# Optimization experiments

Hardware: AMD Instinct MI355X
Metric: run time of the kernel (lower is better)

## Reference

```python
import jax, jax.numpy as jnp
import numpy as np

H = 1024
I = 4096
E = 8
B, S, K = 2, 2048, 2


def setup_inputs() -> dict:
    key = jax.random.key(0)
    k1, k2, k3, k4, k5, k6 = jax.random.split(key, 6)
    x = jax.random.normal(k1, (B, S, H), dtype=jnp.float32)
    expert_indices = jax.random.randint(k2, (B, S, K), 0, E, dtype=jnp.int32)
    expert_weights = jax.random.uniform(k3, (B, S, K), dtype=jnp.float32)
    gate_proj = jax.random.normal(k4, (E, I, H), dtype=jnp.float32) * 0.02
    up_proj = jax.random.normal(k5, (E, I, H), dtype=jnp.float32) * 0.02
    down_proj = jax.random.normal(k6, (E, H, I), dtype=jnp.float32) * 0.02
    return {"x": x, "expert_indices": expert_indices, "expert_weights": expert_weights,
            "gate_proj": gate_proj, "up_proj": up_proj, "down_proj": down_proj}


def reference(x, expert_indices, expert_weights, gate_proj, up_proj, down_proj):
    b, s, h = x.shape
    e = gate_proj.shape[0]
    k = expert_indices.shape[-1]
    xf = x.reshape(-1, h)                       # [N, H]
    idx = expert_indices.reshape(-1, k)         # [N, K]
    wts = expert_weights.reshape(-1, k)         # [N, K]
    # combine[n, e] = sum over slots k with idx[n,k]==e of wts[n,k]
    onehot = jax.nn.one_hot(idx, e, dtype=x.dtype)            # [N, K, E]
    combine = jnp.einsum('nk,nke->ne', wts, onehot)           # [N, E]
    out = jnp.zeros_like(xf)
    # Fixed small unrolled loop over experts (data dims fully vectorized).
    for ei in range(e):
        gate = jax.nn.silu(xf @ gate_proj[ei].T)              # [N, I]
        up = xf @ up_proj[ei].T                               # [N, I]
        out = out + ((gate * up) @ down_proj[ei].T) * combine[:, ei:ei + 1]
    return out.reshape(b, s, h)
```

## Files before the change

### kernel.cpp

```cpp
#include <hip/hip_runtime.h>
#include <hip/hip_bf16.h>
#include <cstdint>

#define HD 1024
#define ID 4096
#define NE 8
#define NTOK 4096
#define NASS 8192
#define NWL 72

typedef unsigned short u16;
typedef __attribute__((ext_vector_type(8))) __bf16 bf16x8;
typedef __attribute__((ext_vector_type(4))) float f32x4;

__device__ __forceinline__ void async16(void* lds, const void* g) {
  __builtin_amdgcn_global_load_lds(
      (const __attribute__((address_space(1))) uint32_t*)g,
      (__attribute__((address_space(3))) uint32_t*)lds, 16, 0, 0);
}

__device__ __forceinline__ u16 f2b(float f) {
  __bf16 h = (__bf16)f;
  return __builtin_bit_cast(u16, h);
}

__device__ __forceinline__ bf16x8 cvt8(const float* p) {
  const float4* q = (const float4*)p;
  float4 a = q[0], b = q[1];
  bf16x8 v;
  v[0] = (__bf16)a.x; v[1] = (__bf16)a.y; v[2] = (__bf16)a.z; v[3] = (__bf16)a.w;
  v[4] = (__bf16)b.x; v[5] = (__bf16)b.y; v[6] = (__bf16)b.z; v[7] = (__bf16)b.w;
  return v;
}

__device__ __forceinline__ void pinned_barrier() {
  __builtin_amdgcn_sched_barrier(0);
  __builtin_amdgcn_s_barrier();
  __builtin_amdgcn_sched_barrier(0);
}

__global__ void k_pre(const float* __restrict__ x, const float* __restrict__ gate,
                      const float* __restrict__ up, u16* __restrict__ xb,
                      u16* __restrict__ wg, u16* __restrict__ wu,
                      float* __restrict__ out) {
  const size_t stride = (size_t)gridDim.x * 256;
  for (size_t v = (size_t)blockIdx.x * 256 + threadIdx.x; v < 8912896ull; v += stride) {
    const float* src; u16* dst; size_t off;
    if (v < 524288ull)        { src = x;    dst = xb; off = v;
      float4 z = {0.f, 0.f, 0.f, 0.f};
      float4* op = (float4*)(out + off * 8);
      op[0] = z; op[1] = z;
    }
    else if (v < 4718592ull)  { src = gate; dst = wg; off = v - 524288ull; }
    else                      { src = up;   dst = wu; off = v - 4718592ull; }
    size_t i8 = off * 8;
    *(bf16x8*)(dst + i8) = cvt8(src + i8);
  }
}

__global__ void k_meta(const int* __restrict__ eidx, int* __restrict__ offsets,
                       int* __restrict__ wl, int* __restrict__ tokl) {
  __shared__ int cnt[NE], offs_s[NE + 1], cur[NE];
  int t = threadIdx.x;
  if (t < NE) cnt[t] = 0;
  __syncthreads();
  for (int i = t; i < NASS; i += 1024) atomicAdd(&cnt[eidx[i]], 1);
  __syncthreads();
  if (t == 0) {
    int s = 0;
    for (int e = 0; e < NE; ++e) { offs_s[e] = s; s += cnt[e]; }
    offs_s[NE] = s;
    int w = 0;
    for (int e = 0; e < NE; ++e)
      for (int mt = 0; mt * 128 < cnt[e]; ++mt) wl[w++] = (e << 16) | mt;
    for (; w < NWL; ++w) wl[w] = -1;
  }
  if (t < NE) cur[t] = 0;
  __syncthreads();
  for (int i = t; i < NASS; i += 1024) {
    int e = eidx[i];
    int p = atomicAdd(&cur[e], 1);
    tokl[offs_s[e] + p] = i;
  }
  if (t <= NE) offsets[t] = offs_s[t];
}

__global__ __launch_bounds__(256, 2) void k_g1(
    const u16* __restrict__ xb, const u16* __restrict__ wg, const u16* __restrict__ wu,
    const float* __restrict__ down, u16* __restrict__ wd,
    const int* __restrict__ offsets, const int* __restrict__ wl,
    const int* __restrict__ tokl, u16* __restrict__ interm) {
  const int bx = blockIdx.x;
  const int t = threadIdx.x;
  if (bx >= 32) {
    int cid = (bx - 32) + 32 * (int)blockIdx.y;
    if (cid < 2048) {
#pragma unroll
      for (int l = 0; l < 8; ++l) {
        size_t i8 = (((size_t)cid * 8 + l) * 256 + t) * 8;
        *(bf16x8*)(wd + i8) = cvt8(down + i8);
      }
    }
    return;
  }
  const int wle = wl[blockIdx.y];
  if (wle < 0) return;
  const int e = wle >> 16;
  const int m0 = (wle & 0xffff) << 7;
  const int offs = offsets[e];
  const int Me = offsets[e + 1] - offs;
  const int n0 = bx * 128;
  const int lane = t & 63, wv = t >> 6;
  const int wm = wv & 1, wn = wv >> 1;

  __shared__ __align__(16) u16 As[2][128 * 32];
  __shared__ __align__(16) u16 Bg[2][128 * 32];
  __shared__ __align__(16) u16 Bu[2][128 * 32];

  const u16* asrc[2];
#pragma unroll
  for (int p = 0; p < 2; ++p) {
    int c = p * 256 + t;
    int r = c >> 2, c8 = (c & 3) * 8;
    int row = m0 + r; if (row > Me - 1) row = Me - 1;
    asrc[p] = xb + (size_t)(tokl[offs + row] >> 1) * HD + c8;
  }
  const u16 *bgsrc[2], *busrc[2];
#pragma unroll
  for (int p = 0; p < 2; ++p) {
    int c = p * 256 + t;
    int r = c >> 2, c8 = (c & 3) * 8;
    size_t boff = ((size_t)e * ID + n0 + r) * HD + c8;
    bgsrc[p] = wg + boff;
    busrc[p] = wu + boff;
  }

#define STAGE1(b, ks)                                                           \
  {                                                                             \
    _Pragma("unroll") for (int p = 0; p < 2; ++p) {                             \
      async16((char*)As[b] + (p * 256 + wv * 64) * 16, asrc[p] + (ks) * 32);    \
      async16((char*)Bg[b] + (p * 256 + wv * 64) * 16, bgsrc[p] + (ks) * 32);   \
      async16((char*)Bu[b] + (p * 256 + wv * 64) * 16, busrc[p] + (ks) * 32);   \
    }                                                                           \
  }

  f32x4 accg[4][4], accu[4][4];
#pragma unroll
  for (int mi = 0; mi < 4; ++mi)
#pragma unroll
    for (int ni = 0; ni < 4; ++ni) {
      accg[mi][ni] = (f32x4){0.f, 0.f, 0.f, 0.f};
      accu[mi][ni] = (f32x4){0.f, 0.f, 0.f, 0.f};
    }

  STAGE1(0, 0);

  const int lrow = lane & 15, lk = (lane >> 4) * 8;
#pragma unroll 1
  for (int ks = 0; ks < HD / 32; ++ks) {
    const int curb = ks & 1;
    if (ks < HD / 32 - 1) {
      STAGE1(curb ^ 1, ks + 1);
      asm volatile("s_waitcnt vmcnt(6)" ::: "memory");
    } else {
      asm volatile("s_waitcnt vmcnt(0)" ::: "memory");
    }
    pinned_barrier();
    bf16x8 af[4], bg[4], bu[4];
#pragma unroll
    for (int mi = 0; mi < 4; ++mi)
      af[mi] = *(const bf16x8*)&As[curb][(wm * 64 + mi * 16 + lrow) * 32 + lk];
#pragma unroll
    for (int ni = 0; ni < 4; ++ni) {
      bg[ni] = *(const bf16x8*)&Bg[curb][(wn * 64 + ni * 16 + lrow) * 32 + lk];
      bu[ni] = *(const bf16x8*)&Bu[curb][(wn * 64 + ni * 16 + lrow) * 32 + lk];
    }
#pragma unroll
    for (int mi = 0; mi < 4; ++mi)
#pragma unroll
      for (int ni = 0; ni < 4; ++ni) {
        accg[mi][ni] = __builtin_amdgcn_mfma_f32_16x16x32_bf16(af[mi], bg[ni], accg[mi][ni], 0, 0, 0);
        accu[mi][ni] = __builtin_amdgcn_mfma_f32_16x16x32_bf16(af[mi], bu[ni], accu[mi][ni], 0, 0, 0);
      }
    pinned_barrier();
  }
#undef STAGE1

#pragma unroll
  for (int mi = 0; mi < 4; ++mi) {
    int rb = wm * 64 + mi * 16 + (lane >> 4) * 4;
#pragma unroll
    for (int ni = 0; ni < 4; ++ni) {
      int col = n0 + wn * 64 + ni * 16 + (lane & 15);
#pragma unroll
      for (int j = 0; j < 4; ++j) {
        int row = m0 + rb + j;
        if (row < Me) {
          float g = accg[mi][ni][j], u = accu[mi][ni][j];
          float s = g / (1.f + __expf(-g));
          interm[(size_t)(offs + row) * ID + col] = f2b(s * u);
        }
      }
    }
  }
}

__global__ __launch_bounds__(256, 2) void k_g2(
    const u16* __restrict__ interm, const u16* __restrict__ wd,
    const int* __restrict__ offsets, const int* __restrict__ wl,
    const int* __restrict__ tokl, const float* __restrict__ ewt,
    float* __restrict__ out) {
  const int wle = wl[blockIdx.y];
  if (wle < 0) return;
  const int e = wle >> 16;
  const int m0 = (wle & 0xffff) << 7;
  const int offs = offsets[e];
  const int Me = offsets[e + 1] - offs;
  const int n0 = blockIdx.x * 256;
  const int t = threadIdx.x, lane = t & 63, wv = t >> 6;
  const int wm = wv & 1, wn = wv >> 1;

  __shared__ __align__(16) u16 As[2][128 * 32];
  __shared__ __align__(16) u16 Bs[2][256 * 32];

  const u16* asrc[2];
#pragma unroll
  for (int p = 0; p < 2; ++p) {
    int c = p * 256 + t;
    int r = c >> 2, c8 = (c & 3) * 8;
    int row = m0 + r; if (row > Me - 1) row = Me - 1;
    asrc[p] = interm + (size_t)(offs + row) * ID + c8;
  }
  const u16* bsrc[4];
#pragma unroll
  for (int p = 0; p < 4; ++p) {
    int c = p * 256 + t;
    int r = c >> 2, c8 = (c & 3) * 8;
    bsrc[p] = wd + ((size_t)e * HD + n0 + r) * ID + c8;
  }

#define STAGE2(b, ks)                                                           \
  {                                                                             \
    _Pragma("unroll") for (int p = 0; p < 2; ++p)                               \
      async16((char*)As[b] + (p * 256 + wv * 64) * 16, asrc[p] + (ks) * 32);    \
    _Pragma("unroll") for (int p = 0; p < 4; ++p)                               \
      async16((char*)Bs[b] + (p * 256 + wv * 64) * 16, bsrc[p] + (ks) * 32);    \
  }

  f32x4 acc[4][8];
#pragma unroll
  for (int mi = 0; mi < 4; ++mi)
#pragma unroll
    for (int ni = 0; ni < 8; ++ni) acc[mi][ni] = (f32x4){0.f, 0.f, 0.f, 0.f};

  STAGE2(0, 0);

  const int lrow = lane & 15, lk = (lane >> 4) * 8;
#pragma unroll 1
  for (int ks = 0; ks < ID / 32; ++ks) {
    const int curb = ks & 1;
    if (ks < ID / 32 - 1) {
      STAGE2(curb ^ 1, ks + 1);
      asm volatile("s_waitcnt vmcnt(6)" ::: "memory");
    } else {
      asm volatile("s_waitcnt vmcnt(0)" ::: "memory");
    }
    pinned_barrier();
    bf16x8 af[4], bfr[8];
#pragma unroll
    for (int mi = 0; mi < 4; ++mi)
      af[mi] = *(const bf16x8*)&As[curb][(wm * 64 + mi * 16 + lrow) * 32 + lk];
#pragma unroll
    for (int ni = 0; ni < 8; ++ni)
      bfr[ni] = *(const bf16x8*)&Bs[curb][(wn * 128 + ni * 16 + lrow) * 32 + lk];
#pragma unroll
    for (int mi = 0; mi < 4; ++mi)
#pragma unroll
      for (int ni = 0; ni < 8; ++ni)
        acc[mi][ni] = __builtin_amdgcn_mfma_f32_16x16x32_bf16(af[mi], bfr[ni], acc[mi][ni], 0, 0, 0);
    pinned_barrier();
  }
#undef STAGE2

#pragma unroll
  for (int mi = 0; mi < 4; ++mi) {
    int rb = wm * 64 + mi * 16 + (lane >> 4) * 4;
#pragma unroll
    for (int j = 0; j < 4; ++j) {
      int row = m0 + rb + j;
      if (row < Me) {
        int aid = tokl[offs + row];
        float w = ewt[aid];
        float* orow = out + (size_t)(aid >> 1) * HD;
#pragma unroll
        for (int ni = 0; ni < 8; ++ni) {
          int col = n0 + wn * 128 + ni * 16 + (lane & 15);
          atomicAdd(orow + col, w * acc[mi][ni][j]);
        }
      }
    }
  }
}

extern "C" void kernel_launch(void* const* d_in, const int* in_sizes, int n_in,
                              void* d_out, int out_size, void* d_ws, size_t ws_size,
                              hipStream_t stream) {
  const float* x    = (const float*)d_in[0];
  const int*   eidx = (const int*)d_in[1];
  const float* ewt  = (const float*)d_in[2];
  const float* gate = (const float*)d_in[3];
  const float* up   = (const float*)d_in[4];
  const float* down = (const float*)d_in[5];
  float* out = (float*)d_out;
  char* ws = (char*)d_ws;

  constexpr size_t OFF_INTERM = 0;
  constexpr size_t OFF_XB     = 67108864;
  constexpr size_t OFF_META   = 75497472;
  constexpr size_t OFF_TOK    = 75498496;
  constexpr size_t OFF_WD     = 75531264;
  constexpr size_t OFF_WG     = 142640128;
  constexpr size_t OFF_WU     = 209748992;

  u16* interm  = (u16*)(ws + OFF_INTERM);
  u16* xb      = (u16*)(ws + OFF_XB);
  int* offsets = (int*)(ws + OFF_META);
  int* wl      = (int*)(ws + OFF_META + 64);
  int* tokl    = (int*)(ws + OFF_TOK);
  u16* wd      = (u16*)(ws + OFF_WD);
  u16* wg      = (u16*)(ws + OFF_WG);
  u16* wu      = (u16*)(ws + OFF_WU);

  k_pre<<<dim3(2048), dim3(256), 0, stream>>>(x, gate, up, xb, wg, wu, out);
  k_meta<<<dim3(1), dim3(1024), 0, stream>>>(eidx, offsets, wl, tokl);
  k_g1<<<dim3(64, NWL), dim3(256), 0, stream>>>(xb, wg, wu, down, wd, offsets, wl, tokl, interm);
  k_g2<<<dim3(HD / 256, NWL), dim3(256), 0, stream>>>(interm, wd, offsets, wl, tokl, ewt, out);
}
```

Measured before the change: 463.9 us.

## Restructure gate/up GEMM to 512 threads, BK=64, swizzled LDS and split MFMA phases

The fused gate/up GEMM kernel now runs 512-thread blocks (8 waves in a 2x4 grid, each computing 64x32), and its K step grows from 32 to 64 with double-buffered LDS. The LDS layout uses an XOR swizzle on 16-byte chunks to avoid bank conflicts, and each K step is split into four barrier-separated MFMA phases with s_setprio raised around the math. The down-projection conversion side-path is re-indexed for the larger block. This aims to raise MFMA utilisation and cut LDS conflicts and per-iteration overhead, at the cost of doubling LDS to 96KB per block, which may limit occupancy, and adding more barriers per K step.

```diff
diff --git a/kernel.cpp b/kernel.cpp
--- a/kernel.cpp
+++ b/kernel.cpp
@@ -38,6 +38,8 @@
   __builtin_amdgcn_s_barrier();
   __builtin_amdgcn_sched_barrier(0);
 }
+
+#define LIDX(row, c8) ((row) * 64 + ((((c8) ^ ((row) & 7))) << 3))
 
 __global__ void k_pre(const float* __restrict__ x, const float* __restrict__ gate,
                       const float* __restrict__ up, u16* __restrict__ xb,
@@ -85,7 +87,7 @@
   if (t <= NE) offsets[t] = offs_s[t];
 }
 
-__global__ __launch_bounds__(256, 2) void k_g1(
+__global__ __launch_bounds__(512, 2) void k_g1(
     const u16* __restrict__ xb, const u16* __restrict__ wg, const u16* __restrict__ wu,
     const float* __restrict__ down, u16* __restrict__ wd,
     const int* __restrict__ offsets, const int* __restrict__ wl,
@@ -94,10 +96,10 @@
   const int t = threadIdx.x;
   if (bx >= 32) {
     int cid = (bx - 32) + 32 * (int)blockIdx.y;
-    if (cid < 2048) {
+    if (cid < 1024) {
 #pragma unroll
       for (int l = 0; l < 8; ++l) {
-        size_t i8 = (((size_t)cid * 8 + l) * 256 + t) * 8;
+        size_t i8 = (((size_t)cid * 8 + l) * 512 + t) * 8;
         *(bf16x8*)(wd + i8) = cvt8(down + i8);
       }
     }
@@ -111,77 +113,115 @@
   const int Me = offsets[e + 1] - offs;
   const int n0 = bx * 128;
   const int lane = t & 63, wv = t >> 6;
-  const int wm = wv & 1, wn = wv >> 1;
-
-  __shared__ __align__(16) u16 As[2][128 * 32];
-  __shared__ __align__(16) u16 Bg[2][128 * 32];
-  __shared__ __align__(16) u16 Bu[2][128 * 32];
+  const int wm = wv >> 2, wn = wv & 3;
+
+  __shared__ __align__(16) u16 As[2][128 * 64];
+  __shared__ __align__(16) u16 Bg[2][128 * 64];
+  __shared__ __align__(16) u16 Bu[2][128 * 64];
 
   const u16* asrc[2];
+  const u16 *bgsrc[2], *busrc[2];
 #pragma unroll
   for (int p = 0; p < 2; ++p) {
-    int c = p * 256 + t;
-    int r = c >> 2, c8 = (c & 3) * 8;
-    int row = m0 + r; if (row > Me - 1) row = Me - 1;
-    asrc[p] = xb + (size_t)(tokl[offs + row] >> 1) * HD + c8;
-  }
-  const u16 *bgsrc[2], *busrc[2];
-#pragma unroll
-  for (int p = 0; p < 2; ++p) {
-    int c = p * 256 + t;
-    int r = c >> 2, c8 = (c & 3) * 8;
-    size_t boff = ((size_t)e * ID + n0 + r) * HD + c8;
+    int c = p * 512 + t;
+    int row = c >> 3;
+    int col8 = (c & 7) ^ (row & 7);
+    int arow = m0 + row; if (arow > Me - 1) arow = Me - 1;
+    asrc[p] = xb + (size_t)(tokl[offs + arow] >> 1) * HD + col8 * 8;
+    size_t boff = ((size_t)e * ID + n0 + row) * HD + col8 * 8;
     bgsrc[p] = wg + boff;
     busrc[p] = wu + boff;
   }
 
-#define STAGE1(b, ks)                                                           \
+#define STAGE1(b, kt)                                                           \
   {                                                                             \
     _Pragma("unroll") for (int p = 0; p < 2; ++p) {                             \
-      async16((char*)As[b] + (p * 256 + wv * 64) * 16, asrc[p] + (ks) * 32);    \
-      async16((char*)Bg[b] + (p * 256 + wv * 64) * 16, bgsrc[p] + (ks) * 32);   \
-      async16((char*)Bu[b] + (p * 256 + wv * 64) * 16, busrc[p] + (ks) * 32);   \
+      async16((char*)As[b] + (p * 512 + wv * 64) * 16, asrc[p] + (kt) * 64);    \
+      async16((char*)Bg[b] + (p * 512 + wv * 64) * 16, bgsrc[p] + (kt) * 64);   \
+      async16((char*)Bu[b] + (p * 512 + wv * 64) * 16, busrc[p] + (kt) * 64);   \
     }                                                                           \
   }
 
-  f32x4 accg[4][4], accu[4][4];
+  f32x4 accg[4][2], accu[4][2];
 #pragma unroll
   for (int mi = 0; mi < 4; ++mi)
 #pragma unroll
-    for (int ni = 0; ni < 4; ++ni) {
+    for (int ni = 0; ni < 2; ++ni) {
       accg[mi][ni] = (f32x4){0.f, 0.f, 0.f, 0.f};
       accu[mi][ni] = (f32x4){0.f, 0.f, 0.f, 0.f};
     }
 
   STAGE1(0, 0);
 
-  const int lrow = lane & 15, lk = (lane >> 4) * 8;
+  const int lr = lane & 15, hi = lane >> 4;
 #pragma unroll 1
-  for (int ks = 0; ks < HD / 32; ++ks) {
-    const int curb = ks & 1;
-    if (ks < HD / 32 - 1) {
-      STAGE1(curb ^ 1, ks + 1);
+  for (int kt = 0; kt < HD / 64; ++kt) {
+    const int cur = kt & 1;
+    if (kt < HD / 64 - 1) {
+      STAGE1(cur ^ 1, kt + 1);
       asm volatile("s_waitcnt vmcnt(6)" ::: "memory");
     } else {
       asm volatile("s_waitcnt vmcnt(0)" ::: "memory");
     }
     pinned_barrier();
-    bf16x8 af[4], bg[4], bu[4];
-#pragma unroll
-    for (int mi = 0; mi < 4; ++mi)
-      af[mi] = *(const bf16x8*)&As[curb][(wm * 64 + mi * 16 + lrow) * 32 + lk];
-#pragma unroll
-    for (int ni = 0; ni < 4; ++ni) {
-      bg[ni] = *(const bf16x8*)&Bg[curb][(wn * 64 + ni * 16 + lrow) * 32 + lk];
-      bu[ni] = *(const bf16x8*)&Bu[curb][(wn * 64 + ni * 16 + lrow) * 32 + lk];
-    }
-#pragma unroll
-    for (int mi = 0; mi < 4; ++mi)
-#pragma unroll
-      for (int ni = 0; ni < 4; ++ni) {
-        accg[mi][ni] = __builtin_amdgcn_mfma_f32_16x16x32_bf16(af[mi], bg[ni], accg[mi][ni], 0, 0, 0);
-        accu[mi][ni] = __builtin_amdgcn_mfma_f32_16x16x32_bf16(af[mi], bu[ni], accu[mi][ni], 0, 0, 0);
-      }
+
+    const u16* A = As[cur];
+    const u16* G = Bg[cur];
+    const u16* U = Bu[cur];
+    bf16x8 af0[4], af1[4], b0[2], b1[2];
+
+#pragma unroll
+    for (int mi = 0; mi < 4; ++mi)
+      af0[mi] = *(const bf16x8*)&A[LIDX(wm * 64 + mi * 16 + lr, hi)];
+#pragma unroll
+    for (int ni = 0; ni < 2; ++ni)
+      b0[ni] = *(const bf16x8*)&G[LIDX(wn * 32 + ni * 16 + lr, hi)];
+    __builtin_amdgcn_s_setprio(1);
+#pragma unroll
+    for (int mi = 0; mi < 4; ++mi)
+#pragma unroll
+      for (int ni = 0; ni < 2; ++ni)
+        accg[mi][ni] = __builtin_amdgcn_mfma_f32_16x16x32_bf16(af0[mi], b0[ni], accg[mi][ni], 0, 0, 0);
+    __builtin_amdgcn_s_setprio(0);
+    pinned_barrier();
+
+#pragma unroll
+    for (int ni = 0; ni < 2; ++ni)
+      b1[ni] = *(const bf16x8*)&U[LIDX(wn * 32 + ni * 16 + lr, hi)];
+    __builtin_amdgcn_s_setprio(1);
+#pragma unroll
+    for (int mi = 0; mi < 4; ++mi)
+#pragma unroll
+      for (int ni = 0; ni < 2; ++ni)
+        accu[mi][ni] = __builtin_amdgcn_mfma_f32_16x16x32_bf16(af0[mi], b1[ni], accu[mi][ni], 0, 0, 0);
+    __builtin_amdgcn_s_setprio(0);
+    pinned_barrier();
+
+#pragma unroll
+    for (int mi = 0; mi < 4; ++mi)
+      af1[mi] = *(const bf16x8*)&A[LIDX(wm * 64 + mi * 16 + lr, 4 + hi)];
+#pragma unroll
+    for (int ni = 0; ni < 2; ++ni)
+      b0[ni] = *(const bf16x8*)&G[LIDX(wn * 32 + ni * 16 + lr, 4 + hi)];
+    __builtin_amdgcn_s_setprio(1);
+#pragma unroll
+    for (int mi = 0; mi < 4; ++mi)
+#pragma unroll
+      for (int ni = 0; ni < 2; ++ni)
+        accg[mi][ni] = __builtin_amdgcn_mfma_f32_16x16x32_bf16(af1[mi], b0[ni], accg[mi][ni], 0, 0, 0);
+    __builtin_amdgcn_s_setprio(0);
+    pinned_barrier();
+
+#pragma unroll
+    for (int ni = 0; ni < 2; ++ni)
+      b1[ni] = *(const bf16x8*)&U[LIDX(wn * 32 + ni * 16 + lr, 4 + hi)];
+    __builtin_amdgcn_s_setprio(1);
+#pragma unroll
+    for (int mi = 0; mi < 4; ++mi)
+#pragma unroll
+      for (int ni = 0; ni < 2; ++ni)
+        accu[mi][ni] = __builtin_amdgcn_mfma_f32_16x16x32_bf16(af1[mi], b1[ni], accu[mi][ni], 0, 0, 0);
+    __builtin_amdgcn_s_setprio(0);
     pinned_barrier();
   }
 #undef STAGE1
@@ -190,8 +230,8 @@
   for (int mi = 0; mi < 4; ++mi) {
     int rb = wm * 64 + mi * 16 + (lane >> 4) * 4;
 #pragma unroll
-    for (int ni = 0; ni < 4; ++ni) {
-      int col = n0 + wn * 64 + ni * 16 + (lane & 15);
+    for (int ni = 0; ni < 2; ++ni) {
+      int col = n0 + wn * 32 + ni * 16 + (lane & 15);
 #pragma unroll
       for (int j = 0; j < 4; ++j) {
         int row = m0 + rb + j;
@@ -333,6 +373,6 @@
 
   k_pre<<<dim3(2048), dim3(256), 0, stream>>>(x, gate, up, xb, wg, wu, out);
   k_meta<<<dim3(1), dim3(1024), 0, stream>>>(eidx, offsets, wl, tokl);
-  k_g1<<<dim3(64, NWL), dim3(256), 0, stream>>>(xb, wg, wu, down, wd, offsets, wl, tokl, interm);
+  k_g1<<<dim3(64, NWL), dim3(512), 0, stream>>>(xb, wg, wu, down, wd, offsets, wl, tokl, interm);
   k_g2<<<dim3(HD / 256, NWL), dim3(256), 0, stream>>>(interm, wd, offsets, wl, tokl, ewt, out);
 }
```

Result: slower. 547.8 us (+18.1%).

## Replace work list with 1D grid interleaving experts and down-proj conversion blocks

Applied to the files above, without the earlier changes.

Removes the serial work-list construction in the metadata kernel and maps a flat 1D block index to (expert, m-tile, n-tile) with the expert as the fastest-varying index. In the first GEMM kernel, down-projection conversion blocks are interleaved with GEMM blocks (5 GEMM chunks to 4 convert chunks) instead of being tacked onto the right half of the grid. The aim is to spread expert work across CUs for better load balance and weight locality, and to overlap the memory-bound conversion with compute. In exchange it assumes at most 10 m-tiles (1280 tokens) per expert, and blocks for empty tiles exit early.

```diff
diff --git a/kernel.cpp b/kernel.cpp
--- a/kernel.cpp
+++ b/kernel.cpp
@@ -7,7 +7,6 @@
 #define NE 8
 #define NTOK 4096
 #define NASS 8192
-#define NWL 72
 
 typedef unsigned short u16;
 typedef __attribute__((ext_vector_type(8))) __bf16 bf16x8;
@@ -59,7 +58,7 @@
 }
 
 __global__ void k_meta(const int* __restrict__ eidx, int* __restrict__ offsets,
-                       int* __restrict__ wl, int* __restrict__ tokl) {
+                       int* __restrict__ tokl) {
   __shared__ int cnt[NE], offs_s[NE + 1], cur[NE];
   int t = threadIdx.x;
   if (t < NE) cnt[t] = 0;
@@ -70,10 +69,6 @@
     int s = 0;
     for (int e = 0; e < NE; ++e) { offs_s[e] = s; s += cnt[e]; }
     offs_s[NE] = s;
-    int w = 0;
-    for (int e = 0; e < NE; ++e)
-      for (int mt = 0; mt * 128 < cnt[e]; ++mt) wl[w++] = (e << 16) | mt;
-    for (; w < NWL; ++w) wl[w] = -1;
   }
   if (t < NE) cur[t] = 0;
   __syncthreads();
@@ -88,28 +83,29 @@
 __global__ __launch_bounds__(256, 2) void k_g1(
     const u16* __restrict__ xb, const u16* __restrict__ wg, const u16* __restrict__ wu,
     const float* __restrict__ down, u16* __restrict__ wd,
-    const int* __restrict__ offsets, const int* __restrict__ wl,
-    const int* __restrict__ tokl, u16* __restrict__ interm) {
-  const int bx = blockIdx.x;
+    const int* __restrict__ offsets, const int* __restrict__ tokl,
+    u16* __restrict__ interm) {
   const int t = threadIdx.x;
-  if (bx >= 32) {
-    int cid = (bx - 32) + 32 * (int)blockIdx.y;
-    if (cid < 2048) {
-#pragma unroll
-      for (int l = 0; l < 8; ++l) {
-        size_t i8 = (((size_t)cid * 8 + l) * 256 + t) * 8;
-        *(bf16x8*)(wd + i8) = cvt8(down + i8);
-      }
+  const int L = blockIdx.x;
+  const int chunk = L >> 3, xid = L & 7;
+  const int m9 = chunk % 9, d9 = chunk / 9;
+  if (m9 >= 5) {
+    int cid = (d9 * 4 + (m9 - 5)) * 8 + xid;
+#pragma unroll
+    for (int l = 0; l < 8; ++l) {
+      size_t i8 = (((size_t)cid * 8 + l) * 256 + t) * 8;
+      *(bf16x8*)(wd + i8) = cvt8(down + i8);
     }
     return;
   }
-  const int wle = wl[blockIdx.y];
-  if (wle < 0) return;
-  const int e = wle >> 16;
-  const int m0 = (wle & 0xffff) << 7;
+  const int e = xid;
+  const int slot = d9 * 5 + m9;
+  const int nb = slot / 10, mt = slot % 10;
   const int offs = offsets[e];
   const int Me = offsets[e + 1] - offs;
-  const int n0 = bx * 128;
+  const int m0 = mt << 7;
+  if (m0 >= Me) return;
+  const int n0 = nb << 7;
   const int lane = t & 63, wv = t >> 6;
   const int wm = wv & 1, wn = wv >> 1;
 
@@ -207,16 +203,17 @@
 
 __global__ __launch_bounds__(256, 2) void k_g2(
     const u16* __restrict__ interm, const u16* __restrict__ wd,
-    const int* __restrict__ offsets, const int* __restrict__ wl,
-    const int* __restrict__ tokl, const float* __restrict__ ewt,
-    float* __restrict__ out) {
-  const int wle = wl[blockIdx.y];
-  if (wle < 0) return;
-  const int e = wle >> 16;
-  const int m0 = (wle & 0xffff) << 7;
+    const int* __restrict__ offsets, const int* __restrict__ tokl,
+    const float* __restrict__ ewt, float* __restrict__ out) {
+  const int L = blockIdx.x;
+  const int e = L & 7;
+  const int slot = L >> 3;
+  const int nb = slot / 10, mt = slot % 10;
   const int offs = offsets[e];
   const int Me = offsets[e + 1] - offs;
-  const int n0 = blockIdx.x * 256;
+  const int m0 = mt << 7;
+  if (m0 >= Me) return;
+  const int n0 = nb << 8;
   const int t = threadIdx.x, lane = t & 63, wv = t >> 6;
   const int wm = wv & 1, wn = wv >> 1;
 
@@ -325,14 +322,13 @@
   u16* interm  = (u16*)(ws + OFF_INTERM);
   u16* xb      = (u16*)(ws + OFF_XB);
   int* offsets = (int*)(ws + OFF_META);
-  int* wl      = (int*)(ws + OFF_META + 64);
   int* tokl    = (int*)(ws + OFF_TOK);
   u16* wd      = (u16*)(ws + OFF_WD);
   u16* wg      = (u16*)(ws + OFF_WG);
   u16* wu      = (u16*)(ws + OFF_WU);
 
   k_pre<<<dim3(2048), dim3(256), 0, stream>>>(x, gate, up, xb, wg, wu, out);
-  k_meta<<<dim3(1), dim3(1024), 0, stream>>>(eidx, offsets, wl, tokl);
-  k_g1<<<dim3(64, NWL), dim3(256), 0, stream>>>(xb, wg, wu, down, wd, offsets, wl, tokl, interm);
-  k_g2<<<dim3(HD / 256, NWL), dim3(256), 0, stream>>>(interm, wd, offsets, wl, tokl, ewt, out);
-}
+  k_meta<<<dim3(1), dim3(1024), 0, stream>>>(eidx, offsets, tokl);
+  k_g1<<<dim3(4608), dim3(256), 0, stream>>>(xb, wg, wu, down, wd, offsets, tokl, interm);
+  k_g2<<<dim3(320), dim3(256), 0, stream>>>(interm, wd, offsets, tokl, ewt, out);
+}
```

Measured after the change: 479.8 us. 1.03x slower.

## Enlarge first grouped GEMM M-tile to 256 rows with 512-thread blocks

Applied to the files above, without the earlier changes.

The gate/up grouped GEMM now uses 256-row token tiles per block with 8 waves instead of 128-row tiles with 4 waves, so each gate/up weight tile loaded into LDS is reused across twice as many tokens. A separate work list with 256-row granularity is built for this kernel while the down-projection kernel keeps its 128-row list, and the fused down-weight conversion is remapped to 512 threads. This lowers weight traffic from global memory and the number of blocks, at the cost of more LDS per block, possibly lower occupancy, and more padding waste in partially filled tiles.

```diff
diff --git a/kernel.cpp b/kernel.cpp
--- a/kernel.cpp
+++ b/kernel.cpp
@@ -7,7 +7,8 @@
 #define NE 8
 #define NTOK 4096
 #define NASS 8192
-#define NWL 72
+#define NWL1 48
+#define NWL2 72
 
 typedef unsigned short u16;
 typedef __attribute__((ext_vector_type(8))) __bf16 bf16x8;
@@ -59,7 +60,8 @@
 }
 
 __global__ void k_meta(const int* __restrict__ eidx, int* __restrict__ offsets,
-                       int* __restrict__ wl, int* __restrict__ tokl) {
+                       int* __restrict__ wl1, int* __restrict__ wl2,
+                       int* __restrict__ tokl) {
   __shared__ int cnt[NE], offs_s[NE + 1], cur[NE];
   int t = threadIdx.x;
   if (t < NE) cnt[t] = 0;
@@ -72,8 +74,12 @@
     offs_s[NE] = s;
     int w = 0;
     for (int e = 0; e < NE; ++e)
-      for (int mt = 0; mt * 128 < cnt[e]; ++mt) wl[w++] = (e << 16) | mt;
-    for (; w < NWL; ++w) wl[w] = -1;
+      for (int mt = 0; mt * 256 < cnt[e] && w < NWL1; ++mt) wl1[w++] = (e << 16) | mt;
+    for (; w < NWL1; ++w) wl1[w] = -1;
+    int w2 = 0;
+    for (int e = 0; e < NE; ++e)
+      for (int mt = 0; mt * 128 < cnt[e] && w2 < NWL2; ++mt) wl2[w2++] = (e << 16) | mt;
+    for (; w2 < NWL2; ++w2) wl2[w2] = -1;
   }
   if (t < NE) cur[t] = 0;
   __syncthreads();
@@ -85,63 +91,56 @@
   if (t <= NE) offsets[t] = offs_s[t];
 }
 
-__global__ __launch_bounds__(256, 2) void k_g1(
+__global__ __launch_bounds__(512, 2) void k_g1(
     const u16* __restrict__ xb, const u16* __restrict__ wg, const u16* __restrict__ wu,
     const float* __restrict__ down, u16* __restrict__ wd,
-    const int* __restrict__ offsets, const int* __restrict__ wl,
+    const int* __restrict__ offsets, const int* __restrict__ wl1,
     const int* __restrict__ tokl, u16* __restrict__ interm) {
   const int bx = blockIdx.x;
   const int t = threadIdx.x;
   if (bx >= 32) {
     int cid = (bx - 32) + 32 * (int)blockIdx.y;
-    if (cid < 2048) {
+    if (cid < 1024) {
 #pragma unroll
       for (int l = 0; l < 8; ++l) {
-        size_t i8 = (((size_t)cid * 8 + l) * 256 + t) * 8;
+        size_t i8 = (((size_t)cid * 8 + l) * 512 + t) * 8;
         *(bf16x8*)(wd + i8) = cvt8(down + i8);
       }
     }
     return;
   }
-  const int wle = wl[blockIdx.y];
+  const int wle = wl1[blockIdx.y];
   if (wle < 0) return;
   const int e = wle >> 16;
-  const int m0 = (wle & 0xffff) << 7;
+  const int m0 = (wle & 0xffff) << 8;
   const int offs = offsets[e];
   const int Me = offsets[e + 1] - offs;
   const int n0 = bx * 128;
   const int lane = t & 63, wv = t >> 6;
-  const int wm = wv & 1, wn = wv >> 1;
-
-  __shared__ __align__(16) u16 As[2][128 * 32];
+  const int wm = wv >> 1, wn = wv & 1;
+
+  __shared__ __align__(16) u16 As[2][256 * 32];
   __shared__ __align__(16) u16 Bg[2][128 * 32];
   __shared__ __align__(16) u16 Bu[2][128 * 32];
 
   const u16* asrc[2];
 #pragma unroll
   for (int p = 0; p < 2; ++p) {
-    int c = p * 256 + t;
+    int c = p * 512 + t;
     int r = c >> 2, c8 = (c & 3) * 8;
     int row = m0 + r; if (row > Me - 1) row = Me - 1;
     asrc[p] = xb + (size_t)(tokl[offs + row] >> 1) * HD + c8;
   }
-  const u16 *bgsrc[2], *busrc[2];
-#pragma unroll
-  for (int p = 0; p < 2; ++p) {
-    int c = p * 256 + t;
-    int r = c >> 2, c8 = (c & 3) * 8;
-    size_t boff = ((size_t)e * ID + n0 + r) * HD + c8;
-    bgsrc[p] = wg + boff;
-    busrc[p] = wu + boff;
-  }
+  const int br = t >> 2, bc8 = (t & 3) * 8;
+  const u16* bgsrc = wg + ((size_t)e * ID + n0 + br) * HD + bc8;
+  const u16* busrc = wu + ((size_t)e * ID + n0 + br) * HD + bc8;
 
 #define STAGE1(b, ks)                                                           \
   {                                                                             \
-    _Pragma("unroll") for (int p = 0; p < 2; ++p) {                             \
-      async16((char*)As[b] + (p * 256 + wv * 64) * 16, asrc[p] + (ks) * 32);    \
-      async16((char*)Bg[b] + (p * 256 + wv * 64) * 16, bgsrc[p] + (ks) * 32);   \
-      async16((char*)Bu[b] + (p * 256 + wv * 64) * 16, busrc[p] + (ks) * 32);   \
-    }                                                                           \
+    _Pragma("unroll") for (int p = 0; p < 2; ++p)                               \
+      async16((char*)As[b] + (p * 512 + wv * 64) * 16, asrc[p] + (ks) * 32);    \
+    async16((char*)Bg[b] + (wv * 64) * 16, bgsrc + (ks) * 32);                  \
+    async16((char*)Bu[b] + (wv * 64) * 16, busrc + (ks) * 32);                  \
   }
 
   f32x4 accg[4][4], accu[4][4];
@@ -161,7 +160,7 @@
     const int curb = ks & 1;
     if (ks < HD / 32 - 1) {
       STAGE1(curb ^ 1, ks + 1);
-      asm volatile("s_waitcnt vmcnt(6)" ::: "memory");
+      asm volatile("s_waitcnt vmcnt(4)" ::: "memory");
     } else {
       asm volatile("s_waitcnt vmcnt(0)" ::: "memory");
     }
@@ -207,10 +206,10 @@
 
 __global__ __launch_bounds__(256, 2) void k_g2(
     const u16* __restrict__ interm, const u16* __restrict__ wd,
-    const int* __restrict__ offsets, const int* __restrict__ wl,
+    const int* __restrict__ offsets, const int* __restrict__ wl2,
     const int* __restrict__ tokl, const float* __restrict__ ewt,
     float* __restrict__ out) {
-  const int wle = wl[blockIdx.y];
+  const int wle = wl2[blockIdx.y];
   if (wle < 0) return;
   const int e = wle >> 16;
   const int m0 = (wle & 0xffff) << 7;
@@ -325,14 +324,15 @@
   u16* interm  = (u16*)(ws + OFF_INTERM);
   u16* xb      = (u16*)(ws + OFF_XB);
   int* offsets = (int*)(ws + OFF_META);
-  int* wl      = (int*)(ws + OFF_META + 64);
+  int* wl1     = (int*)(ws + OFF_META + 64);
+  int* wl2     = (int*)(ws + OFF_META + 320);
   int* tokl    = (int*)(ws + OFF_TOK);
   u16* wd      = (u16*)(ws + OFF_WD);
   u16* wg      = (u16*)(ws + OFF_WG);
   u16* wu      = (u16*)(ws + OFF_WU);
 
   k_pre<<<dim3(2048), dim3(256), 0, stream>>>(x, gate, up, xb, wg, wu, out);
-  k_meta<<<dim3(1), dim3(1024), 0, stream>>>(eidx, offsets, wl, tokl);
-  k_g1<<<dim3(64, NWL), dim3(256), 0, stream>>>(xb, wg, wu, down, wd, offsets, wl, tokl, interm);
-  k_g2<<<dim3(HD / 256, NWL), dim3(256), 0, stream>>>(interm, wd, offsets, wl, tokl, ewt, out);
-}
+  k_meta<<<dim3(1), dim3(1024), 0, stream>>>(eidx, offsets, wl1, wl2, tokl);
+  k_g1<<<dim3(64, NWL1), dim3(512), 0, stream>>>(xb, wg, wu, down, wd, offsets, wl1, tokl, interm);
+  k_g2<<<dim3(HD / 256, NWL2), dim3(256), 0, stream>>>(interm, wd, offsets, wl2, tokl, ewt, out);
+}
```

Result: slower. 498.1 us (+7.4%).
